# Kernel tuning notes

Measured on AMD Instinct MI355X. Metric: run time of the kernel, lower is better.

Reference implementation:

```python
import jax, jax.numpy as jnp
import numpy as np


def setup_inputs() -> dict:
    key = jax.random.key(0)
    k1, k2 = jax.random.split(key)
    B, D, H, W = 4, 32, 32, 16
    logits = jax.random.normal(k1, (B, D, H, W), dtype=jnp.float32)
    # binary segmentation targets (0/1), cast to float as in the torch module
    targets = jax.random.randint(k2, (B, D, H, W), 0, 2).astype(jnp.float32)
    return {"logits": logits, "targets": targets}


def reference(logits, targets):
    B = logits.shape[0]
    spatial = logits.shape[1:]
    V = int(np.prod(spatial))
    # Voxel coordinates of the full grid (row-major, same order as torch.nonzero).
    grids = jnp.meshgrid(*[jnp.arange(s) for s in spatial], indexing="ij")
    coords = jnp.stack(grids, axis=-1).reshape(V, len(spatial)).astype(jnp.float32)  # [V, ndim]
    # Shared squared pairwise distance matrix between all grid voxels: [V, V].
    # ||p - t||^2 = ||p||^2 + ||t||^2 - 2 p.t ; max over masked pairs then sqrt
    # equals max of cdist over masked pairs (sqrt is monotone).
    sq = jnp.sum(coords * coords, axis=1)  # [V]
    d2 = sq[:, None] + sq[None, :] - 2.0 * (coords @ coords.T)  # [V, V]

    probs = jax.nn.sigmoid(logits).reshape(B, V)
    pmask = probs > 0.5                     # pred foreground voxels  [B, V]
    tmask = targets.reshape(B, V) > 0.5     # target foreground voxels [B, V]
    neg_inf = jnp.float32(-jnp.inf)

    def per_sample(masks):
        pm, tm = masks
        # max over target voxels for each pred voxel, then max over pred voxels.
        # Note: torch code takes max over the FULL cdist matrix in both
        # directions; both equal the max pairwise distance, so one pass suffices.
        row = jnp.max(jnp.where(tm[None, :], d2, neg_inf), axis=1)  # [V]
        m = jnp.max(jnp.where(pm, row, neg_inf))
        valid = jnp.any(pm) & jnp.any(tm)
        return jnp.where(valid, jnp.sqrt(jnp.maximum(m, 0.0)), jnp.inf)

    # sequential over batch to avoid materializing [B, V, V]
    hd = jax.lax.map(per_sample, (pmask, tmask))  # [B]
    return jnp.mean(hd)
```

## Files before the change

### kernel.cpp

```cpp
#include <hip/hip_runtime.h>
#include <math.h>

#define NB 4
#define ND 32
#define NH 32
#define NW 16
#define CPS (ND * NH)
#define VPS (CPS * NW)
#define NBLK 256
#define PC 128
#define TC 128

__global__ __launch_bounds__(512) void hd_one(
    const float* __restrict__ logits, const float* __restrict__ targets,
    int* bmax, unsigned* cnt, float* __restrict__ out) {
    __shared__ int2 s_pe[PC];
    __shared__ int2 s_te[TC];
    __shared__ int s_red[8];
    __shared__ int s_win;

    int bid = blockIdx.x;
    int s = bid >> 6;
    int pchunk = (bid >> 3) & 7;
    int tchunk = bid & 7;
    int tid = threadIdx.x;

    if (tid < 256) {
        bool isp = tid < PC;
        int lc = tid & (PC - 1);
        int col = (isp ? pchunk : tchunk) * PC + lc;
        const float4* p4 =
            (const float4*)((isp ? logits : targets) + s * VPS + col * NW);
        float thr = isp ? 0.0f : 0.5f;
        unsigned msk = 0;
#pragma unroll
        for (int j = 0; j < 4; ++j) {
            float4 v = p4[j];
            msk |= (v.x > thr ? 1u : 0u) << (4 * j);
            msk |= (v.y > thr ? 1u : 0u) << (4 * j + 1);
            msk |= (v.z > thr ? 1u : 0u) << (4 * j + 2);
            msk |= (v.w > thr ? 1u : 0u) << (4 * j + 3);
        }
        int2 e = make_int2(msk ? (__ffs(msk) - 1) : 1000,
                           msk ? (31 - __clz(msk)) : -1);
        if (isp) s_pe[lc] = e; else s_te[lc] = e;
    }
    __syncthreads();

    int lp = tid >> 2;
    int tg = tid & 3;
    int2 pe = s_pe[lp];
    int pcol = pchunk * PC + lp;
    int pd = pcol >> 5, ph = pcol & 31;

    int dd2[4], dh2[8];
#pragma unroll
    for (int k = 0; k < 4; ++k) { int d = pd - (tchunk * 4 + k); dd2[k] = d * d; }
#pragma unroll
    for (int j = 0; j < 8; ++j) { int h = ph - (4 * j + tg); dh2[j] = h * h; }

    int best = -1;
#pragma unroll
    for (int i = 0; i < 32; ++i) {
        int2 te = s_te[tg + 4 * i];
        int q = max(pe.y - te.x, te.y - pe.x);
        int cand = dd2[i >> 3] + dh2[i & 7] + q * q;
        best = (te.y >= 0) ? max(best, cand) : best;
    }
    if (pe.y < 0) best = -1;

#pragma unroll
    for (int m = 32; m >= 1; m >>= 1) best = max(best, __shfl_xor(best, m, 64));
    if ((tid & 63) == 0) s_red[tid >> 6] = best;
    __syncthreads();

    if (tid == 0) {
        int mx = s_red[0];
#pragma unroll
        for (int i = 1; i < 8; ++i) mx = max(mx, s_red[i]);
        __hip_atomic_store(&bmax[bid], mx, __ATOMIC_RELAXED,
                           __HIP_MEMORY_SCOPE_AGENT);
        asm volatile("s_waitcnt vmcnt(0)" ::: "memory");
        unsigned old = atomicAdd(cnt, 1u);
        s_win = (((old + 1u) & (NBLK - 1u)) == 0u) ? 1 : 0;
    }
    __syncthreads();

    if (s_win && tid < 64) {
        int b0 = tid * 4;
        int m0 = __hip_atomic_load(&bmax[b0 + 0], __ATOMIC_RELAXED,
                                   __HIP_MEMORY_SCOPE_AGENT);
        int m1 = __hip_atomic_load(&bmax[b0 + 1], __ATOMIC_RELAXED,
                                   __HIP_MEMORY_SCOPE_AGENT);
        int m2 = __hip_atomic_load(&bmax[b0 + 2], __ATOMIC_RELAXED,
                                   __HIP_MEMORY_SCOPE_AGENT);
        int m3 = __hip_atomic_load(&bmax[b0 + 3], __ATOMIC_RELAXED,
                                   __HIP_MEMORY_SCOPE_AGENT);
        int m = max(max(m0, m1), max(m2, m3));
#pragma unroll
        for (int k = 8; k >= 1; k >>= 1) m = max(m, __shfl_xor(m, k, 64));
        float hd = (m < 0) ? INFINITY : sqrtf((float)m);
        float ssum = __shfl(hd, 0, 64) + __shfl(hd, 16, 64) +
                     __shfl(hd, 32, 64) + __shfl(hd, 48, 64);
        if (tid == 0) out[0] = ssum * (1.0f / NB);
    }
}

extern "C" void kernel_launch(void* const* d_in, const int* in_sizes, int n_in,
                              void* d_out, int out_size, void* d_ws, size_t ws_size,
                              hipStream_t stream) {
    const float* logits  = (const float*)d_in[0];
    const float* targets = (const float*)d_in[1];
    float* out = (float*)d_out;

    int* bmax = (int*)d_ws;
    unsigned* cnt = (unsigned*)((char*)d_ws + NBLK * sizeof(int));

    hd_one<<<NBLK, 512, 0, stream>>>(logits, targets, bmax, cnt, out);
}
```

Measured before the change: 12.43 us.

## Use fewer larger blocks and a two-level atomic counter for final reduction

Cuts the grid from 256 to 64 blocks, with each block covering a 256x256 chunk pair instead of 128x128, so each thread runs 128 inner iterations instead of 32. The single global completion counter becomes per-group counters, each padded onto its own 128-byte slot, plus a final counter, which reduces atomic contention on one address. The aim is lower launch and cross-block synchronisation overhead. The cost is more serial work per thread and fewer blocks to spread across the CUs.

```diff
diff --git a/kernel.cpp b/kernel.cpp
--- a/kernel.cpp
+++ b/kernel.cpp
@@ -7,25 +7,25 @@
 #define NW 16
 #define CPS (ND * NH)
 #define VPS (CPS * NW)
-#define NBLK 256
-#define PC 128
-#define TC 128
+#define NBLK 64
+#define PC 256
+#define TC 256
 
 __global__ __launch_bounds__(512) void hd_one(
     const float* __restrict__ logits, const float* __restrict__ targets,
-    int* bmax, unsigned* cnt, float* __restrict__ out) {
+    int* bmax, unsigned* gcnt, unsigned* fcnt, float* __restrict__ out) {
     __shared__ int2 s_pe[PC];
     __shared__ int2 s_te[TC];
     __shared__ int s_red[8];
     __shared__ int s_win;
 
     int bid = blockIdx.x;
-    int s = bid >> 6;
-    int pchunk = (bid >> 3) & 7;
-    int tchunk = bid & 7;
+    int s = bid >> 4;
+    int pchunk = (bid >> 2) & 3;
+    int tchunk = bid & 3;
     int tid = threadIdx.x;
 
-    if (tid < 256) {
+    {
         bool isp = tid < PC;
         int lc = tid & (PC - 1);
         int col = (isp ? pchunk : tchunk) * PC + lc;
@@ -47,24 +47,24 @@
     }
     __syncthreads();
 
-    int lp = tid >> 2;
-    int tg = tid & 3;
+    int lp = tid >> 1;
+    int tg = tid & 1;
     int2 pe = s_pe[lp];
-    int pcol = pchunk * PC + lp;
-    int pd = pcol >> 5, ph = pcol & 31;
+    int pd = pchunk * 8 + (lp >> 5);
+    int ph = lp & 31;
 
-    int dd2[4], dh2[8];
+    int dd2[8], dh2[16];
 #pragma unroll
-    for (int k = 0; k < 4; ++k) { int d = pd - (tchunk * 4 + k); dd2[k] = d * d; }
+    for (int k = 0; k < 8; ++k) { int d = pd - (tchunk * 8 + k); dd2[k] = d * d; }
 #pragma unroll
-    for (int j = 0; j < 8; ++j) { int h = ph - (4 * j + tg); dh2[j] = h * h; }
+    for (int j = 0; j < 16; ++j) { int h = ph - (2 * j + tg); dh2[j] = h * h; }
 
     int best = -1;
-#pragma unroll
-    for (int i = 0; i < 32; ++i) {
-        int2 te = s_te[tg + 4 * i];
+#pragma unroll 16
+    for (int i = 0; i < 128; ++i) {
+        int2 te = s_te[2 * i + tg];
         int q = max(pe.y - te.x, te.y - pe.x);
-        int cand = dd2[i >> 3] + dh2[i & 7] + q * q;
+        int cand = dd2[i >> 4] + dh2[i & 15] + q * q;
         best = (te.y >= 0) ? max(best, cand) : best;
     }
     if (pe.y < 0) best = -1;
@@ -81,22 +81,21 @@
         __hip_atomic_store(&bmax[bid], mx, __ATOMIC_RELAXED,
                            __HIP_MEMORY_SCOPE_AGENT);
         asm volatile("s_waitcnt vmcnt(0)" ::: "memory");
-        unsigned old = atomicAdd(cnt, 1u);
-        s_win = (((old + 1u) & (NBLK - 1u)) == 0u) ? 1 : 0;
+        int win = 0;
+        int g = bid >> 3;
+        unsigned o1 = atomicAdd(&gcnt[g * 32], 1u);
+        if (((o1 + 1u) & 7u) == 0u) {
+            asm volatile("s_waitcnt vmcnt(0)" ::: "memory");
+            unsigned o2 = atomicAdd(fcnt, 1u);
+            win = (((o2 + 1u) & 7u) == 0u);
+        }
+        s_win = win;
     }
     __syncthreads();
 
     if (s_win && tid < 64) {
-        int b0 = tid * 4;
-        int m0 = __hip_atomic_load(&bmax[b0 + 0], __ATOMIC_RELAXED,
-                                   __HIP_MEMORY_SCOPE_AGENT);
-        int m1 = __hip_atomic_load(&bmax[b0 + 1], __ATOMIC_RELAXED,
-                                   __HIP_MEMORY_SCOPE_AGENT);
-        int m2 = __hip_atomic_load(&bmax[b0 + 2], __ATOMIC_RELAXED,
-                                   __HIP_MEMORY_SCOPE_AGENT);
-        int m3 = __hip_atomic_load(&bmax[b0 + 3], __ATOMIC_RELAXED,
-                                   __HIP_MEMORY_SCOPE_AGENT);
-        int m = max(max(m0, m1), max(m2, m3));
+        int m = __hip_atomic_load(&bmax[tid], __ATOMIC_RELAXED,
+                                  __HIP_MEMORY_SCOPE_AGENT);
 #pragma unroll
         for (int k = 8; k >= 1; k >>= 1) m = max(m, __shfl_xor(m, k, 64));
         float hd = (m < 0) ? INFINITY : sqrtf((float)m);
@@ -113,8 +112,10 @@
     const float* targets = (const float*)d_in[1];
     float* out = (float*)d_out;
 
-    int* bmax = (int*)d_ws;
-    unsigned* cnt = (unsigned*)((char*)d_ws + NBLK * sizeof(int));
+    char* ws = (char*)d_ws;
+    int* bmax = (int*)ws;
+    unsigned* gcnt = (unsigned*)(ws + 512);
+    unsigned* fcnt = (unsigned*)(ws + 512 + 8 * 128);
 
-    hd_one<<<NBLK, 512, 0, stream>>>(logits, targets, bmax, cnt, out);
+    hd_one<<<NBLK, 512, 0, stream>>>(logits, targets, bmax, gcnt, fcnt, out);
 }
```

Result: slower. 29.51 us (+137.4%).
